# Kernel optimization log

Hardware: AMD Instinct MI355X
Metric: run time of the kernel (lower is better)

The kernel has to match this reference:

```python
import jax, jax.numpy as jnp
import numpy as np

N = 100000  # nodes
E = 1600000  # directed edges

_DIMS = [("eg1", 3, 160), ("eg2", 160, 80), ("eg3", 80, 40), ("eg4", 40, 20),
         ("el1", 20, 10), ("el2", 10, 3), ("dl1", 3, 10), ("dl2", 10, 20),
         ("dg1", 20, 40), ("dg2", 40, 80), ("dg3", 80, 160), ("dg4", 160, 3)]


def _lin_init(key, ci, co):
    s = 1.0 / np.sqrt(ci)
    kw, kb = jax.random.split(key)
    w = jax.random.uniform(kw, (ci, co), jnp.float32, -s, s)
    b = jax.random.uniform(kb, (co,), jnp.float32, -s, s)
    return w, b


def setup_inputs():
    key = jax.random.key(0)
    k0, k1, k2 = jax.random.split(key, 3)
    x = jax.random.normal(k0, (N, 3), jnp.float32)
    src = jax.random.randint(k1, (E,), 0, N)
    dst = jax.random.randint(k2, (E,), 0, N)
    edge_index = jnp.stack([src, dst])  # [2, E] int32 indices
    out = {"x": x, "edge_index": edge_index}
    for i, (name, ci, co) in enumerate(_DIMS):
        w, b = _lin_init(jax.random.fold_in(key, i + 10), ci, co)
        out[name + "_w"] = w
        out[name + "_b"] = b
    return out


def _gcn(x, w, b, src, dst, norm):
    # PyG GCNConv: linear transform, then symmetric-normalized scatter-add.
    h = x @ w
    agg = jax.ops.segment_sum(h[src] * norm[:, None], dst, num_segments=N)
    return agg + b


def reference(x, edge_index, eg1_w, eg1_b, eg2_w, eg2_b, eg3_w, eg3_b, eg4_w, eg4_b,
              el1_w, el1_b, el2_w, el2_b, dl1_w, dl1_b, dl2_w, dl2_b,
              dg1_w, dg1_b, dg2_w, dg2_b, dg3_w, dg3_b, dg4_w, dg4_b):
    loops = jnp.arange(N)
    src = jnp.concatenate([edge_index[0], loops])  # add self-loops (PyG default)
    dst = jnp.concatenate([edge_index[1], loops])
    deg = jax.ops.segment_sum(jnp.ones(src.shape[0], x.dtype), dst, num_segments=N)
    dis = jnp.where(deg > 0, jax.lax.rsqrt(deg), 0.0)
    norm = dis[src] * dis[dst]  # D^-1/2 A D^-1/2 edge weights
    relu = jax.nn.relu
    h = relu(_gcn(x, eg1_w, eg1_b, src, dst, norm))
    h = relu(_gcn(h, eg2_w, eg2_b, src, dst, norm))
    h = relu(_gcn(h, eg3_w, eg3_b, src, dst, norm))
    h = relu(_gcn(h, eg4_w, eg4_b, src, dst, norm))
    h = relu(h @ el1_w + el1_b)
    h = h @ el2_w + el2_b  # latent [N, 3]
    h = relu(h @ dl1_w + dl1_b)
    h = relu(h @ dl2_w + dl2_b)
    h = relu(_gcn(h, dg1_w, dg1_b, src, dst, norm))
    h = relu(_gcn(h, dg2_w, dg2_b, src, dst, norm))
    h = relu(_gcn(h, dg3_w, dg3_b, src, dst, norm))
    h = jnp.tanh(_gcn(h, dg4_w, dg4_b, src, dst, norm))
    return h
```

## Files before the change

### kernel.cpp

```cpp
#include <hip/hip_runtime.h>
#include <hip/hip_fp16.h>
#include <math.h>

#define BS 256
static constexpr int NN = 100000;
static constexpr int EE = 1600000;
static constexpr int BUCKET_SH = 7;
static constexpr int NBUCKET = (NN + 127) >> BUCKET_SH;
static constexpr int NB_PART = 256;
static constexpr int CHUNK = EE / NB_PART;
static constexpr int NP_ = NBUCKET * NB_PART;
static constexpr int SCAN_ELEMS = 1024;
static constexpr int NPB = (NP_ + SCAN_ELEMS - 1) / SCAN_ELEMS;

static inline int cdiv(long long a, int b) { return (int)((a + b - 1) / b); }

typedef _Float16 half8 __attribute__((ext_vector_type(8)));
typedef float f32x4 __attribute__((ext_vector_type(4)));

template <int ACT>
__device__ __forceinline__ float act_f(float v) {
    if (ACT == 1) return fmaxf(v, 0.0f);
    if (ACT == 2) return tanhf(v);
    return v;
}

__device__ __forceinline__ unsigned short h16(float v) {
    return __half_as_ushort(__float2half(v));
}
__device__ __forceinline__ unsigned pack2h(float a, float b) {
    return (unsigned)h16(a) | ((unsigned)h16(b) << 16);
}
__device__ __forceinline__ float4 cvt4h(uint2 r) {
    float2 fa = __half22float2(*(const __half2*)&r.x);
    float2 fb = __half22float2(*(const __half2*)&r.y);
    return make_float4(fa.x, fa.y, fb.x, fb.y);
}
__device__ __forceinline__ void acc8h(uint4 r, float4& a, float4& b) {
    float2 f0 = __half22float2(*(const __half2*)&r.x);
    float2 f1 = __half22float2(*(const __half2*)&r.y);
    float2 f2 = __half22float2(*(const __half2*)&r.z);
    float2 f3 = __half22float2(*(const __half2*)&r.w);
    a.x += f0.x; a.y += f0.y; a.z += f1.x; a.w += f1.y;
    b.x += f2.x; b.y += f2.y; b.z += f3.x; b.w += f3.y;
}
__device__ __forceinline__ void addrow8(uint4 r, float* h) {
    float2 f0 = __half22float2(*(const __half2*)&r.x);
    float2 f1 = __half22float2(*(const __half2*)&r.y);
    float2 f2 = __half22float2(*(const __half2*)&r.z);
    float2 f3 = __half22float2(*(const __half2*)&r.w);
    h[0] += f0.x; h[1] += f0.y; h[2] += f1.x; h[3] += f1.y;
    h[4] += f2.x; h[5] += f2.y; h[6] += f3.x; h[7] += f3.y;
}
__device__ __forceinline__ void addrow4(uint2 r, float* h) {
    float2 f0 = __half22float2(*(const __half2*)&r.x);
    float2 f1 = __half22float2(*(const __half2*)&r.y);
    h[0] += f0.x; h[1] += f0.y; h[2] += f1.x; h[3] += f1.y;
}

template <int OUTM>
__device__ __forceinline__ void store1(float* out, size_t idx, float v, float dn) {
    if (OUTM == 0) out[idx] = v;
    else if (OUTM == 1) out[idx] = v * dn;
    else if (OUTM == 2) ((unsigned short*)out)[idx] = h16(v * dn);
    else ((unsigned short*)out)[idx] = h16(v);
}

__global__ __launch_bounds__(256) void k_hist(const int* __restrict__ dst,
                                              int* __restrict__ part_cnt) {
    __shared__ int h[NBUCKET];
    int b = blockIdx.x;
    for (int j = threadIdx.x; j < NBUCKET; j += 256) h[j] = 0;
    __syncthreads();
    int e0 = b * CHUNK;
    for (int k = threadIdx.x; k < CHUNK; k += 256)
        atomicAdd(&h[dst[e0 + k] >> BUCKET_SH], 1);
    __syncthreads();
    for (int j = threadIdx.x; j < NBUCKET; j += 256)
        part_cnt[j * NB_PART + b] = h[j];
}

__global__ void k_scanA(const int* __restrict__ in, int* __restrict__ outp,
                        int* __restrict__ bsums) {
    __shared__ int lds[BS];
    int base = blockIdx.x * SCAN_ELEMS;
    int t = threadIdx.x;
    int v[4];
    int s = 0;
#pragma unroll
    for (int j = 0; j < 4; ++j) {
        int idx = base + t * 4 + j;
        v[j] = (idx < NP_) ? in[idx] : 0;
        s += v[j];
    }
    lds[t] = s;
    __syncthreads();
    for (int off = 1; off < BS; off <<= 1) {
        int add = (t >= off) ? lds[t - off] : 0;
        __syncthreads();
        lds[t] += add;
        __syncthreads();
    }
    int run = lds[t] - s;
    if (t == BS - 1) bsums[blockIdx.x] = lds[BS - 1];
#pragma unroll
    for (int j = 0; j < 4; ++j) {
        int idx = base + t * 4 + j;
        if (idx < NP_) outp[idx] = run;
        run += v[j];
    }
}

__global__ void k_scanB(int* __restrict__ bsums) {
    if (threadIdx.x == 0 && blockIdx.x == 0) {
        int acc = 0;
        for (int i = 0; i < NPB; ++i) {
            int t = bsums[i];
            bsums[i] = acc;
            acc += t;
        }
    }
}

__global__ void k_scanC(int* __restrict__ outp, const int* __restrict__ bsums,
                        int* __restrict__ bbase) {
    int i = blockIdx.x * BS + threadIdx.x;
    if (i < NP_) {
        int v = outp[i] + bsums[i / SCAN_ELEMS];
        outp[i] = v;
        if ((i & (NB_PART - 1)) == 0) bbase[i / NB_PART] = v;
    }
    if (i == 0) bbase[NBUCKET] = EE;
}

__global__ __launch_bounds__(256) void k_part(const int* __restrict__ src,
                                              const int* __restrict__ dst,
                                              const int* __restrict__ scan_out,
                                              unsigned* __restrict__ epb) {
    __shared__ int cur[NBUCKET];
    int b = blockIdx.x;
    for (int j = threadIdx.x; j < NBUCKET; j += 256) cur[j] = scan_out[j * NB_PART + b];
    __syncthreads();
    int e0 = b * CHUNK;
    for (int k = threadIdx.x; k < CHUNK; k += 256) {
        int e = e0 + k;
        int d = dst[e];
        int s = src[e];
        int pos = atomicAdd(&cur[d >> BUCKET_SH], 1);
        epb[pos] = ((unsigned)(d & ((1 << BUCKET_SH) - 1)) << 17) | (unsigned)s;
    }
}

__global__ __launch_bounds__(256) void k_fine2(const int* __restrict__ bbase,
                                               const unsigned* __restrict__ epb,
                                               int* __restrict__ eidx,
                                               int* __restrict__ rowptr,
                                               float* __restrict__ dis) {
    __shared__ int hcnt[1 << BUCKET_SH];
    __shared__ int hoff[1 << BUCKET_SH];
    int b = blockIdx.x;
    int n0 = b << BUCKET_SH;
    int nloc = min(1 << BUCKET_SH, NN - n0);
    int t = threadIdx.x;
    if (t < (1 << BUCKET_SH)) hcnt[t] = 0;
    __syncthreads();
    int es = bbase[b], ee = bbase[b + 1];
    for (int k = es + t; k < ee; k += 256) atomicAdd(&hcnt[epb[k] >> 17], 1);
    __syncthreads();
    if (t < (1 << BUCKET_SH)) hoff[t] = hcnt[t];
    __syncthreads();
    for (int off = 1; off < (1 << BUCKET_SH); off <<= 1) {
        int add = (t >= off && t < (1 << BUCKET_SH)) ? hoff[t - off] : 0;
        __syncthreads();
        if (t < (1 << BUCKET_SH)) hoff[t] += add;
        __syncthreads();
    }
    if (t < nloc) {
        int excl = hoff[t] - hcnt[t];
        rowptr[n0 + t] = es + excl;
        dis[n0 + t] = rsqrtf((float)(hcnt[t] + 1));
    }
    __syncthreads();
    if (t < (1 << BUCKET_SH)) hoff[t] = es + hoff[t] - hcnt[t];
    __syncthreads();
    for (int k = es + t; k < ee; k += 256) {
        unsigned p = epb[k];
        int pos = atomicAdd(&hoff[p >> 17], 1);
        eidx[pos] = (int)(p & 0x1FFFFu);
    }
    if (b == NBUCKET - 1 && t == 0) rowptr[NN] = EE;
}

template <int K, int N>
__device__ __forceinline__ void wconv(const float* __restrict__ w, _Float16* __restrict__ wh, int i) {
    constexpr int NT = (N + 15) / 16;
    constexpr int NPAD = NT * 16;
    int k = i / NPAD, n = i % NPAD;
    float v = (k < K && n < N) ? w[k * N + n] : 0.0f;
    wh[((size_t)(k >> 3) * NPAD + n) * 8 + (k & 7)] = (_Float16)v;
}

__global__ void k_wprep_all(const float* __restrict__ w1, const float* __restrict__ w2,
                            const float* __restrict__ w3, const float* __restrict__ w4,
                            _Float16* __restrict__ o1, _Float16* __restrict__ o2,
                            _Float16* __restrict__ o3, _Float16* __restrict__ o4) {
    int i = blockIdx.x * 256 + threadIdx.x;
    if (i < 12800) wconv<160, 80>(w1, o1, i);
    else if (i < 17408) wconv<80, 40>(w2, o2, i - 12800);
    else if (i < 22528) wconv<40, 80>(w3, o3, i - 17408);
    else if (i < 37888) wconv<80, 160>(w4, o4, i - 22528);
}

__global__ void k_gather3x(const float* __restrict__ x, const int* __restrict__ rowptr,
                           const int* __restrict__ eidx, const float* __restrict__ dis,
                           float* __restrict__ out) {
    int n = blockIdx.x * BS + threadIdx.x;
    if (n >= NN) return;
    float dn = dis[n];
    float a0 = x[(size_t)n * 3 + 0] * dn;
    float a1 = x[(size_t)n * 3 + 1] * dn;
    float a2 = x[(size_t)n * 3 + 2] * dn;
    int rs = rowptr[n], re = rowptr[n + 1];
    int k = rs;
    for (; k + 2 <= re; k += 2) {
        int s0 = eidx[k], s1 = eidx[k + 1];
        float d0 = dis[s0], d1 = dis[s1];
        const float* q0 = x + (size_t)s0 * 3;
        const float* q1 = x + (size_t)s1 * 3;
        a0 += q0[0] * d0 + q1[0] * d1;
        a1 += q0[1] * d0 + q1[1] * d1;
        a2 += q0[2] * d0 + q1[2] * d1;
    }
    for (; k < re; ++k) {
        int s = eidx[k];
        float ds = dis[s];
        const float* q = x + (size_t)s * 3;
        a0 += q[0] * ds; a1 += q[1] * ds; a2 += q[2] * ds;
    }
    float* op = out + (size_t)n * 3;
    op[0] = a0 * dn; op[1] = a1 * dn; op[2] = a2 * dn;
}

template <int ACT, bool HASB>
__global__ void k_gather3d(const float* __restrict__ g, const int* __restrict__ rowptr,
                           const int* __restrict__ eidx, const float* __restrict__ dis,
                           const float* __restrict__ b, float* __restrict__ out) {
    int n = blockIdx.x * BS + threadIdx.x;
    if (n >= NN) return;
    const float* gp = g + (size_t)n * 3;
    float a0 = gp[0], a1 = gp[1], a2 = gp[2];
    int rs = rowptr[n], re = rowptr[n + 1];
    int k = rs;
    for (; k + 4 <= re; k += 4) {
        const float* q0 = g + (size_t)eidx[k + 0] * 3;
        const float* q1 = g + (size_t)eidx[k + 1] * 3;
        const float* q2 = g + (size_t)eidx[k + 2] * 3;
        const float* q3 = g + (size_t)eidx[k + 3] * 3;
        a0 += (q0[0] + q1[0]) + (q2[0] + q3[0]);
        a1 += (q0[1] + q1[1]) + (q2[1] + q3[1]);
        a2 += (q0[2] + q1[2]) + (q2[2] + q3[2]);
    }
    for (; k < re; ++k) {
        const float* gq = g + (size_t)eidx[k] * 3;
        a0 += gq[0]; a1 += gq[1]; a2 += gq[2];
    }
    float dn = dis[n];
    a0 *= dn; a1 *= dn; a2 *= dn;
    if (HASB) { a0 += b[0]; a1 += b[1]; a2 += b[2]; }
    float* op = out + (size_t)n * 3;
    op[0] = act_f<ACT>(a0);
    op[1] = act_f<ACT>(a1);
    op[2] = act_f<ACT>(a2);
}

__global__ __launch_bounds__(256) void k_eg12(const float* __restrict__ a3,
                                              const float* __restrict__ w1,
                                              const float* __restrict__ b1,
                                              const _Float16* __restrict__ wh2,
                                              unsigned short* __restrict__ out,
                                              const float* __restrict__ dis) {
    constexpr int SP = 168;
    __shared__ _Float16 Al[64 * SP];
    __shared__ float xs[192];
    __shared__ float w1s[480];
    __shared__ float b1s[160];
    const int tid = threadIdx.x;
    const int n0 = blockIdx.x * 64;
    for (int i = tid; i < 192; i += 256) {
        int n = n0 + i / 3;
        xs[i] = (n < NN) ? a3[(size_t)n0 * 3 + i] : 0.0f;
    }
    for (int i = tid; i < 480; i += 256) w1s[i] = w1[i];
    if (tid < 160) b1s[tid] = b1[tid];
    __syncthreads();
    for (int i = tid; i < 64 * 160; i += 256) {
        int r = i / 160, c = i % 160;
        float v = b1s[c] + xs[r * 3 + 0] * w1s[c] + xs[r * 3 + 1] * w1s[160 + c] +
                  xs[r * 3 + 2] * w1s[320 + c];
        Al[r * SP + c] = (_Float16)fmaxf(v, 0.0f);
    }
    __syncthreads();
    const int wave = tid >> 6, lane = tid & 63;
    const int lm = lane & 15, quad = lane >> 4;
    f32x4 acc[5];
#pragma unroll
    for (int t = 0; t < 5; ++t) acc[t] = (f32x4){0.f, 0.f, 0.f, 0.f};
    const int arow = wave * 16 + lm;
#pragma unroll
    for (int kc = 0; kc < 5; ++kc) {
        half8 a = *(const half8*)&Al[arow * SP + kc * 32 + quad * 8];
#pragma unroll
        for (int t = 0; t < 5; ++t) {
            half8 bf = *(const half8*)&wh2[((size_t)(kc * 4 + quad) * 80 + t * 16 + lm) * 8];
            acc[t] = __builtin_amdgcn_mfma_f32_16x16x32_f16(a, bf, acc[t], 0, 0, 0);
        }
    }
#pragma unroll
    for (int r = 0; r < 4; ++r) {
        int orow = n0 + wave * 16 + quad * 4 + r;
        if (orow < NN) {
            float dn = dis[orow];
#pragma unroll
            for (int t = 0; t < 5; ++t) {
                int col = t * 16 + lm;
                out[(size_t)orow * 80 + col] = h16(acc[t][r] * dn);
            }
        }
    }
}

template <int CIN, int COUT, bool GHASB, int GACT, bool MHASB, int MACT, int OUTM>
__global__ __launch_bounds__(256) void k_gmfma(const unsigned short* __restrict__ gin,
                                               const int* __restrict__ rowptr,
                                               const int* __restrict__ eidx,
                                               const float* __restrict__ dis,
                                               const float* __restrict__ gbias,
                                               const _Float16* __restrict__ wh,
                                               const float* __restrict__ mbias,
                                               unsigned short* __restrict__ out) {
    static_assert(CIN % 8 == 0, "CIN%8");
    constexpr int V = CIN / 8;
    constexpr int SP = CIN + 8;
    constexpr int KP = (CIN + 31) & ~31;
    constexpr int KC = KP / 32;
    constexpr int NT = (COUT + 15) / 16;
    constexpr int NPAD = NT * 16;
    __shared__ _Float16 Al[64 * SP];
    const int tid = threadIdx.x;
    const int n0 = blockIdx.x * 64;
    const uint4* g4 = (const uint4*)gin;

    for (int i = tid; i < 64 * V; i += 256) {
        int r = i / V, c8 = i % V;
        int n = n0 + r;
        half8 hv = (half8)(_Float16)0;
        if (n < NN) {
            float4 aA = make_float4(0.f, 0.f, 0.f, 0.f);
            float4 aB = make_float4(0.f, 0.f, 0.f, 0.f);
            acc8h(g4[(size_t)n * V + c8], aA, aB);
            int rs = rowptr[n], re = rowptr[n + 1];
            int k = rs;
            for (; k + 4 <= re; k += 4) {
                int s0 = eidx[k + 0], s1 = eidx[k + 1], s2 = eidx[k + 2], s3 = eidx[k + 3];
                uint4 r0 = g4[(size_t)s0 * V + c8];
                uint4 r1 = g4[(size_t)s1 * V + c8];
                uint4 r2 = g4[(size_t)s2 * V + c8];
                uint4 r3 = g4[(size_t)s3 * V + c8];
                acc8h(r0, aA, aB);
                acc8h(r1, aA, aB);
                acc8h(r2, aA, aB);
                acc8h(r3, aA, aB);
            }
            for (; k < re; ++k) acc8h(g4[(size_t)eidx[k] * V + c8], aA, aB);
            float dn = dis[n];
            aA.x *= dn; aA.y *= dn; aA.z *= dn; aA.w *= dn;
            aB.x *= dn; aB.y *= dn; aB.z *= dn; aB.w *= dn;
            if (GHASB) {
                float4 b0 = ((const float4*)gbias)[c8 * 2 + 0];
                float4 b1 = ((const float4*)gbias)[c8 * 2 + 1];
                aA.x += b0.x; aA.y += b0.y; aA.z += b0.z; aA.w += b0.w;
                aB.x += b1.x; aB.y += b1.y; aB.z += b1.z; aB.w += b1.w;
            }
            if (GACT == 1) {
                aA.x = fmaxf(aA.x, 0.f); aA.y = fmaxf(aA.y, 0.f);
                aA.z = fmaxf(aA.z, 0.f); aA.w = fmaxf(aA.w, 0.f);
                aB.x = fmaxf(aB.x, 0.f); aB.y = fmaxf(aB.y, 0.f);
                aB.z = fmaxf(aB.z, 0.f); aB.w = fmaxf(aB.w, 0.f);
            }
            hv[0] = (_Float16)aA.x; hv[1] = (_Float16)aA.y;
            hv[2] = (_Float16)aA.z; hv[3] = (_Float16)aA.w;
            hv[4] = (_Float16)aB.x; hv[5] = (_Float16)aB.y;
            hv[6] = (_Float16)aB.z; hv[7] = (_Float16)aB.w;
        }
        *(half8*)&Al[r * SP + c8 * 8] = hv;
    }
    __syncthreads();

    const int wave = tid >> 6, lane = tid & 63;
    const int lm = lane & 15, quad = lane >> 4;
    f32x4 acc[NT];
#pragma unroll
    for (int t = 0; t < NT; ++t) acc[t] = (f32x4){0.f, 0.f, 0.f, 0.f};
    const int arow = wave * 16 + lm;
#pragma unroll
    for (int kc = 0; kc < KC; ++kc) {
        int k0 = kc * 32 + quad * 8;
        half8 a = (half8)(_Float16)0;
        if (k0 < CIN) a = *(const half8*)&Al[arow * SP + k0];
#pragma unroll
        for (int t = 0; t < NT; ++t) {
            half8 bf = *(const half8*)&wh[((size_t)(kc * 4 + quad) * NPAD + t * 16 + lm) * 8];
            acc[t] = __builtin_amdgcn_mfma_f32_16x16x32_f16(a, bf, acc[t], 0, 0, 0);
        }
    }
    float bb[NT];
#pragma unroll
    for (int t = 0; t < NT; ++t) {
        int col = t * 16 + lm;
        bb[t] = (MHASB && col < COUT) ? mbias[col] : 0.0f;
    }
#pragma unroll
    for (int r = 0; r < 4; ++r) {
        int orow = n0 + wave * 16 + quad * 4 + r;
        if (orow < NN) {
            float dn = (OUTM == 2) ? dis[orow] : 1.0f;
#pragma unroll
            for (int t = 0; t < NT; ++t) {
                int col = t * 16 + lm;
                if (col < COUT) {
                    float v = act_f<MACT>(acc[t][r] + bb[t]);
                    if (OUTM == 2) v *= dn;
                    out[(size_t)orow * COUT + col] = h16(v);
                }
            }
        }
    }
}

__global__ __launch_bounds__(256) void k_g40mm(const unsigned short* __restrict__ gin,
                                               const int* __restrict__ rowptr,
                                               const int* __restrict__ eidx,
                                               const float* __restrict__ dis,
                                               const float* __restrict__ gb,
                                               const float* __restrict__ w,
                                               unsigned short* __restrict__ out) {
    __shared__ float wS[800];
    __shared__ float bS[40];
    int tid = threadIdx.x;
    for (int i = tid; i < 800; i += 256) wS[i] = w[i];
    if (tid < 40) bS[tid] = gb[tid];
    __syncthreads();
    int n = blockIdx.x * 256 + tid;
    if (n >= NN) return;
    const uint4* g4 = (const uint4*)gin;
    float h[40];
#pragma unroll
    for (int i = 0; i < 40; ++i) h[i] = 0.0f;
#pragma unroll
    for (int c8 = 0; c8 < 5; ++c8) addrow8(g4[(size_t)n * 5 + c8], &h[c8 * 8]);
    int rs = rowptr[n], re = rowptr[n + 1];
    int k = rs;
    for (; k + 2 <= re; k += 2) {
        int s0 = eidx[k], s1 = eidx[k + 1];
#pragma unroll
        for (int c8 = 0; c8 < 5; ++c8) {
            uint4 r0 = g4[(size_t)s0 * 5 + c8];
            uint4 r1 = g4[(size_t)s1 * 5 + c8];
            addrow8(r0, &h[c8 * 8]);
            addrow8(r1, &h[c8 * 8]);
        }
    }
    for (; k < re; ++k) {
        int s = eidx[k];
#pragma unroll
        for (int c8 = 0; c8 < 5; ++c8) addrow8(g4[(size_t)s * 5 + c8], &h[c8 * 8]);
    }
    float dn = dis[n];
#pragma unroll
    for (int i = 0; i < 40; ++i) h[i] = fmaxf(h[i] * dn + bS[i], 0.0f);
    float z[20];
#pragma unroll
    for (int j = 0; j < 20; ++j) z[j] = 0.0f;
#pragma unroll
    for (int i = 0; i < 40; ++i) {
        float hv = h[i];
#pragma unroll
        for (int j = 0; j < 20; ++j) z[j] = fmaf(hv, wS[i * 20 + j], z[j]);
    }
    uint2* gp = (uint2*)out + (size_t)n * 5;
#pragma unroll
    for (int q = 0; q < 5; ++q) {
        uint2 u;
        u.x = pack2h(z[q * 4 + 0] * dn, z[q * 4 + 1] * dn);
        u.y = pack2h(z[q * 4 + 2] * dn, z[q * 4 + 3] * dn);
        gp[q] = u;
    }
}

__global__ __launch_bounds__(256) void k_g20_latent(const unsigned short* __restrict__ gin,
                                                    const int* __restrict__ rowptr,
                                                    const int* __restrict__ eidx,
                                                    const float* __restrict__ dis,
                                                    const float* __restrict__ gb,
                                                    const float* __restrict__ el1_w, const float* __restrict__ el1_b,
                                                    const float* __restrict__ el2_w, const float* __restrict__ el2_b,
                                                    const float* __restrict__ dl1_w, const float* __restrict__ dl1_b,
                                                    const float* __restrict__ dl2_w, const float* __restrict__ dl2_b,
                                                    unsigned short* __restrict__ out) {
    __shared__ float w1[200], b1[10], w2[30], b2[3], w3[30], b3[10], w4[200], b4[20], bg[20];
    int t = threadIdx.x;
    if (t < 200) w1[t] = el1_w[t];
    if (t < 10) b1[t] = el1_b[t];
    if (t < 30) w2[t] = el2_w[t];
    if (t < 3) b2[t] = el2_b[t];
    if (t < 30) w3[t] = dl1_w[t];
    if (t < 10) b3[t] = dl1_b[t];
    if (t < 200) w4[t] = dl2_w[t];
    if (t < 20) b4[t] = dl2_b[t];
    if (t >= 220 && t < 240) bg[t - 220] = gb[t - 220];
    __syncthreads();
    int n = blockIdx.x * 256 + t;
    if (n >= NN) return;
    const uint2* g2 = (const uint2*)gin;
    float h0[20];
#pragma unroll
    for (int i = 0; i < 20; ++i) h0[i] = 0.0f;
#pragma unroll
    for (int c4 = 0; c4 < 5; ++c4) addrow4(g2[(size_t)n * 5 + c4], &h0[c4 * 4]);
    int rs = rowptr[n], re = rowptr[n + 1];
    int k = rs;
    for (; k + 4 <= re; k += 4) {
        int s0 = eidx[k], s1 = eidx[k + 1], s2 = eidx[k + 2], s3 = eidx[k + 3];
#pragma unroll
        for (int c4 = 0; c4 < 5; ++c4) {
            uint2 r0 = g2[(size_t)s0 * 5 + c4];
            uint2 r1 = g2[(size_t)s1 * 5 + c4];
            uint2 r2 = g2[(size_t)s2 * 5 + c4];
            uint2 r3 = g2[(size_t)s3 * 5 + c4];
            addrow4(r0, &h0[c4 * 4]);
            addrow4(r1, &h0[c4 * 4]);
            addrow4(r2, &h0[c4 * 4]);
            addrow4(r3, &h0[c4 * 4]);
        }
    }
    for (; k < re; ++k) {
        int s = eidx[k];
#pragma unroll
        for (int c4 = 0; c4 < 5; ++c4) addrow4(g2[(size_t)s * 5 + c4], &h0[c4 * 4]);
    }
    float dn = dis[n];
#pragma unroll
    for (int i = 0; i < 20; ++i) h0[i] = fmaxf(h0[i] * dn + bg[i], 0.0f);
    float a1[10];
#pragma unroll
    for (int j = 0; j < 10; ++j) {
        float s = b1[j];
#pragma unroll
        for (int i = 0; i < 20; ++i) s = fmaf(h0[i], w1[i * 10 + j], s);
        a1[j] = fmaxf(s, 0.0f);
    }
    float a2[3];
#pragma unroll
    for (int j = 0; j < 3; ++j) {
        float s = b2[j];
#pragma unroll
        for (int i = 0; i < 10; ++i) s = fmaf(a1[i], w2[i * 3 + j], s);
        a2[j] = s;
    }
    float a3[10];
#pragma unroll
    for (int j = 0; j < 10; ++j) {
        float s = b3[j];
#pragma unroll
        for (int i = 0; i < 3; ++i) s = fmaf(a2[i], w3[i * 10 + j], s);
        a3[j] = fmaxf(s, 0.0f);
    }
    uint2* gp = (uint2*)out + (size_t)n * 5;
#pragma unroll
    for (int v = 0; v < 5; ++v) {
        float o[4];
#pragma unroll
        for (int q = 0; q < 4; ++q) {
            int j = v * 4 + q;
            float s = b4[j];
#pragma unroll
            for (int i = 0; i < 10; ++i) s = fmaf(a3[i], w4[i * 20 + j], s);
            o[q] = fmaxf(s, 0.0f) * dn;
        }
        uint2 u;
        u.x = pack2h(o[0], o[1]);
        u.y = pack2h(o[2], o[3]);
        gp[v] = u;
    }
}

__global__ __launch_bounds__(256) void k_g20_mm(const unsigned short* __restrict__ gin,
                                                const int* __restrict__ rowptr,
                                                const int* __restrict__ eidx,
                                                const float* __restrict__ dis,
                                                const float* __restrict__ w,
                                                const float* __restrict__ b,
                                                unsigned short* __restrict__ out) {
    __shared__ float wS[800];
    __shared__ float bS[40];
    int tid = threadIdx.x;
    for (int i = tid; i < 800; i += 256) wS[i] = w[i];
    if (tid < 40) bS[tid] = b[tid];
    __syncthreads();
    int n = blockIdx.x * 256 + tid;
    if (n >= NN) return;
    const uint2* g2 = (const uint2*)gin;
    float h[20];
#pragma unroll
    for (int i = 0; i < 20; ++i) h[i] = 0.0f;
#pragma unroll
    for (int c4 = 0; c4 < 5; ++c4) addrow4(g2[(size_t)n * 5 + c4], &h[c4 * 4]);
    int rs = rowptr[n], re = rowptr[n + 1];
    int k = rs;
    for (; k + 4 <= re; k += 4) {
        int s0 = eidx[k], s1 = eidx[k + 1], s2 = eidx[k + 2], s3 = eidx[k + 3];
#pragma unroll
        for (int c4 = 0; c4 < 5; ++c4) {
            uint2 r0 = g2[(size_t)s0 * 5 + c4];
            uint2 r1 = g2[(size_t)s1 * 5 + c4];
            uint2 r2 = g2[(size_t)s2 * 5 + c4];
            uint2 r3 = g2[(size_t)s3 * 5 + c4];
            addrow4(r0, &h[c4 * 4]);
            addrow4(r1, &h[c4 * 4]);
            addrow4(r2, &h[c4 * 4]);
            addrow4(r3, &h[c4 * 4]);
        }
    }
    for (; k < re; ++k) {
        int s = eidx[k];
#pragma unroll
        for (int c4 = 0; c4 < 5; ++c4) addrow4(g2[(size_t)s * 5 + c4], &h[c4 * 4]);
    }
    float dn = dis[n];
#pragma unroll
    for (int i = 0; i < 20; ++i) h[i] *= dn;
    float z[40];
#pragma unroll
    for (int j = 0; j < 40; ++j) z[j] = bS[j];
#pragma unroll
    for (int i = 0; i < 20; ++i) {
        float hv = h[i];
#pragma unroll
        for (int j = 0; j < 40; ++j) z[j] = fmaf(hv, wS[i * 40 + j], z[j]);
    }
    uint2* gp = (uint2*)out + (size_t)n * 10;
#pragma unroll
    for (int q = 0; q < 10; ++q) {
        float z0 = fmaxf(z[q * 4 + 0], 0.f) * dn;
        float z1 = fmaxf(z[q * 4 + 1], 0.f) * dn;
        float z2 = fmaxf(z[q * 4 + 2], 0.f) * dn;
        float z3 = fmaxf(z[q * 4 + 3], 0.f) * dn;
        uint2 u;
        u.x = pack2h(z0, z1);
        u.y = pack2h(z2, z3);
        gp[q] = u;
    }
}

template <int CIN, int COUT, int ACT, bool HASB, int OUTM, bool INH>
__global__ void k_mm_vec(const float* __restrict__ x, const float* __restrict__ w,
                         const float* __restrict__ b, float* __restrict__ out,
                         const float* __restrict__ dis) {
    static_assert(CIN % 4 == 0, "CIN%4");
    constexpr int TM = 8;
    constexpr int CIN4 = CIN / 4;
    constexpr int RG = NN / TM;
    int i = blockIdx.x * BS + threadIdx.x;
    if (i >= RG * COUT) return;
    int c = i % COUT;
    int n0 = (i / COUT) * TM;
    float acc[TM];
    float bb = HASB ? b[c] : 0.0f;
#pragma unroll
    for (int r = 0; r < TM; ++r) acc[r] = bb;
    const float4* x4 = (const float4*)x;
    const uint2* xh = (const uint2*)x;
    for (int k = 0; k < CIN4; ++k) {
        float w0 = w[(4 * k + 0) * COUT + c];
        float w1 = w[(4 * k + 1) * COUT + c];
        float w2 = w[(4 * k + 2) * COUT + c];
        float w3 = w[(4 * k + 3) * COUT + c];
#pragma unroll
        for (int r = 0; r < TM; ++r) {
            float4 xv;
            if (INH) xv = cvt4h(xh[(size_t)(n0 + r) * CIN4 + k]);
            else xv = x4[(size_t)(n0 + r) * CIN4 + k];
            acc[r] = fmaf(xv.x, w0, fmaf(xv.y, w1, fmaf(xv.z, w2, fmaf(xv.w, w3, acc[r]))));
        }
    }
#pragma unroll
    for (int r = 0; r < TM; ++r) {
        int row = n0 + r;
        float dn = (OUTM == 1 || OUTM == 2) ? dis[row] : 0.0f;
        store1<OUTM>(out, (size_t)row * COUT + c, act_f<ACT>(acc[r]), dn);
    }
}

extern "C" void kernel_launch(void* const* d_in, const int* in_sizes, int n_in,
                              void* d_out, int out_size, void* d_ws, size_t ws_size,
                              hipStream_t stream) {
    const float* x = (const float*)d_in[0];
    const int* ei = (const int*)d_in[1];
    const int* src = ei;
    const int* dst = ei + EE;
    const float* eg1_w = (const float*)d_in[2];  const float* eg1_b = (const float*)d_in[3];
    const float* eg2_w = (const float*)d_in[4];  const float* eg2_b = (const float*)d_in[5];
    const float* eg3_w = (const float*)d_in[6];  const float* eg3_b = (const float*)d_in[7];
    const float* eg4_w = (const float*)d_in[8];  const float* eg4_b = (const float*)d_in[9];
    const float* el1_w = (const float*)d_in[10]; const float* el1_b = (const float*)d_in[11];
    const float* el2_w = (const float*)d_in[12]; const float* el2_b = (const float*)d_in[13];
    const float* dl1_w = (const float*)d_in[14]; const float* dl1_b = (const float*)d_in[15];
    const float* dl2_w = (const float*)d_in[16]; const float* dl2_b = (const float*)d_in[17];
    const float* dg1_w = (const float*)d_in[18]; const float* dg1_b = (const float*)d_in[19];
    const float* dg2_w = (const float*)d_in[20]; const float* dg2_b = (const float*)d_in[21];
    const float* dg3_w = (const float*)d_in[22]; const float* dg3_b = (const float*)d_in[23];
    const float* dg4_w = (const float*)d_in[24]; const float* dg4_b = (const float*)d_in[25];
    float* out = (float*)d_out;

    char* ws = (char*)d_ws;
    size_t off = 0;
    auto alloc = [&](size_t bytes) {
        void* p = ws + off;
        off += (bytes + 15) & ~(size_t)15;
        return p;
    };
    int* part_cnt = (int*)alloc(sizeof(int) * NP_);
    int* scan_out = (int*)alloc(sizeof(int) * NP_);
    int* bsums    = (int*)alloc(sizeof(int) * NPB);
    int* bbase    = (int*)alloc(sizeof(int) * (NBUCKET + 1));
    int* rowptr   = (int*)alloc(sizeof(int) * (NN + 1));
    float* dis    = (float*)alloc(sizeof(float) * NN);
    int* eidx     = (int*)alloc(sizeof(int) * EE);
    unsigned* epb = (unsigned*)alloc(sizeof(unsigned) * EE);
    float* A3     = (float*)alloc(sizeof(float) * 3 * (size_t)NN);
    unsigned short* GA = (unsigned short*)alloc(sizeof(unsigned short) * 80 * (size_t)NN);
    unsigned short* GB = (unsigned short*)alloc(sizeof(unsigned short) * 80 * (size_t)NN);
    unsigned short* B160 = (unsigned short*)alloc(sizeof(unsigned short) * 160 * (size_t)NN);
    _Float16* whEg2 = (_Float16*)alloc(sizeof(_Float16) * 12800);
    _Float16* whEg3 = (_Float16*)alloc(sizeof(_Float16) * 4608);
    _Float16* whDg2 = (_Float16*)alloc(sizeof(_Float16) * 5120);
    _Float16* whDg3 = (_Float16*)alloc(sizeof(_Float16) * 15360);

    k_hist<<<NB_PART, 256, 0, stream>>>(dst, part_cnt);
    k_scanA<<<NPB, BS, 0, stream>>>(part_cnt, scan_out, bsums);
    k_scanB<<<1, 64, 0, stream>>>(bsums);
    k_scanC<<<cdiv(NP_, BS), BS, 0, stream>>>(scan_out, bsums, bbase);
    k_part<<<NB_PART, 256, 0, stream>>>(src, dst, scan_out, epb);
    k_fine2<<<NBUCKET, 256, 0, stream>>>(bbase, epb, eidx, rowptr, dis);

    k_wprep_all<<<cdiv(37888, 256), 256, 0, stream>>>(eg2_w, eg3_w, dg2_w, dg3_w,
                                                      whEg2, whEg3, whDg2, whDg3);

    k_gather3x<<<cdiv(NN, BS), BS, 0, stream>>>(x, rowptr, eidx, dis, A3);
    k_eg12<<<cdiv(NN, 64), 256, 0, stream>>>(A3, eg1_w, eg1_b, whEg2, GA, dis);
    k_gmfma<80, 40, true, 1, false, 0, 2><<<cdiv(NN, 64), 256, 0, stream>>>(
        GA, rowptr, eidx, dis, eg2_b, whEg3, nullptr, GB);
    k_g40mm<<<cdiv(NN, 256), 256, 0, stream>>>(GB, rowptr, eidx, dis, eg3_b, eg4_w, GA);
    k_g20_latent<<<cdiv(NN, 256), 256, 0, stream>>>(GA, rowptr, eidx, dis, eg4_b,
        el1_w, el1_b, el2_w, el2_b, dl1_w, dl1_b, dl2_w, dl2_b, GB);
    k_g20_mm<<<cdiv(NN, 256), 256, 0, stream>>>(GB, rowptr, eidx, dis, dg1_w, dg1_b, GA);
    k_gmfma<40, 80, false, 0, true, 1, 2><<<cdiv(NN, 64), 256, 0, stream>>>(
        GA, rowptr, eidx, dis, nullptr, whDg2, dg2_b, GB);
    k_gmfma<80, 160, false, 0, true, 1, 3><<<cdiv(NN, 64), 256, 0, stream>>>(
        GB, rowptr, eidx, dis, nullptr, whDg3, dg3_b, B160);
    k_mm_vec<160, 3, 0, false, 1, true><<<cdiv((NN / 8) * 3LL, BS), BS, 0, stream>>>(
        (const float*)B160, dg4_w, nullptr, A3, dis);
    k_gather3d<2, true><<<cdiv(NN, BS), BS, 0, stream>>>(A3, rowptr, eidx, dis, dg4_b, out);
}
```

Measured before the change: 538.6 us.

## Split fused gather+MFMA kernels into separate gather and matmul kernels

Replaces the fused k_gmfma kernel, which gathered neighbor rows into shared memory and then ran an MFMA matmul, with two kernels. A thread-per-8-channel gather kernel writes the aggregated fp16 features to global memory, and a standalone MFMA matmul kernel reads them back. The aim is better gather parallelism and occupancy, since the fused kernel had few threads per block doing the gather and the matmul waited on a barrier. The cost is an extra global round trip of the intermediate activations and extra kernel launches.

```diff
diff --git a/kernel.cpp b/kernel.cpp
--- a/kernel.cpp
+++ b/kernel.cpp
@@ -273,6 +273,114 @@
     op[2] = act_f<ACT>(a2);
 }
 
+template <int C, int ACT, bool HASB>
+__global__ void k_gatherw(const unsigned short* __restrict__ g, const int* __restrict__ rowptr,
+                          const int* __restrict__ eidx, const float* __restrict__ dis,
+                          const float* __restrict__ b, unsigned short* __restrict__ out) {
+    static_assert(C % 8 == 0, "C%8");
+    constexpr int V = C / 8;
+    int t = blockIdx.x * BS + threadIdx.x;
+    if (t >= NN * V) return;
+    int n = t / V, v = t % V;
+    const uint4* g4 = (const uint4*)g;
+    float4 accA = make_float4(0.f, 0.f, 0.f, 0.f);
+    float4 accB = make_float4(0.f, 0.f, 0.f, 0.f);
+    acc8h(g4[(size_t)n * V + v], accA, accB);
+    int rs = rowptr[n], re = rowptr[n + 1];
+    int k = rs;
+    for (; k + 4 <= re; k += 4) {
+        int s0 = eidx[k + 0], s1 = eidx[k + 1], s2 = eidx[k + 2], s3 = eidx[k + 3];
+        uint4 r0 = g4[(size_t)s0 * V + v];
+        uint4 r1 = g4[(size_t)s1 * V + v];
+        uint4 r2 = g4[(size_t)s2 * V + v];
+        uint4 r3 = g4[(size_t)s3 * V + v];
+        acc8h(r0, accA, accB);
+        acc8h(r1, accA, accB);
+        acc8h(r2, accA, accB);
+        acc8h(r3, accA, accB);
+    }
+    for (; k < re; ++k) {
+        acc8h(g4[(size_t)eidx[k] * V + v], accA, accB);
+    }
+    float dn = dis[n];
+    accA.x *= dn; accA.y *= dn; accA.z *= dn; accA.w *= dn;
+    accB.x *= dn; accB.y *= dn; accB.z *= dn; accB.w *= dn;
+    if (HASB) {
+        float4 b0 = ((const float4*)b)[v * 2 + 0];
+        float4 b1 = ((const float4*)b)[v * 2 + 1];
+        accA.x += b0.x; accA.y += b0.y; accA.z += b0.z; accA.w += b0.w;
+        accB.x += b1.x; accB.y += b1.y; accB.z += b1.z; accB.w += b1.w;
+    }
+    accA.x = act_f<ACT>(accA.x); accA.y = act_f<ACT>(accA.y);
+    accA.z = act_f<ACT>(accA.z); accA.w = act_f<ACT>(accA.w);
+    accB.x = act_f<ACT>(accB.x); accB.y = act_f<ACT>(accB.y);
+    accB.z = act_f<ACT>(accB.z); accB.w = act_f<ACT>(accB.w);
+    uint4 u;
+    u.x = pack2h(accA.x, accA.y);
+    u.y = pack2h(accA.z, accA.w);
+    u.z = pack2h(accB.x, accB.y);
+    u.w = pack2h(accB.z, accB.w);
+    ((uint4*)out)[(size_t)n * V + v] = u;
+}
+
+template <int K, int N, int ACT, bool HASB, int OUTM>
+__global__ __launch_bounds__(256) void k_mfma(const unsigned short* __restrict__ x,
+                                              const _Float16* __restrict__ wh,
+                                              const float* __restrict__ bias,
+                                              unsigned short* __restrict__ out,
+                                              const float* __restrict__ dis) {
+    static_assert(K % 8 == 0, "K%8");
+    constexpr int KP = (K + 31) & ~31;
+    constexpr int KC = KP / 32;
+    constexpr int NT = (N + 15) / 16;
+    constexpr int NPAD = NT * 16;
+    const int wid = blockIdx.x * 4 + (threadIdx.x >> 6);
+    const int lane = threadIdx.x & 63;
+    const int lm = lane & 15;
+    const int quad = lane >> 4;
+    const int arow = wid * 16 + lm;
+
+    f32x4 acc[NT];
+#pragma unroll
+    for (int t = 0; t < NT; ++t) acc[t] = (f32x4){0.f, 0.f, 0.f, 0.f};
+
+    const _Float16* xr = (const _Float16*)x + (size_t)arow * K;
+#pragma unroll
+    for (int kc = 0; kc < KC; ++kc) {
+        int k0 = kc * 32 + quad * 8;
+        half8 a = (half8)(_Float16)0;
+        if (arow < NN && k0 < K) a = *(const half8*)(xr + k0);
+#pragma unroll
+        for (int t = 0; t < NT; ++t) {
+            half8 bf = *(const half8*)&wh[((size_t)(kc * 4 + quad) * NPAD + t * 16 + lm) * 8];
+            acc[t] = __builtin_amdgcn_mfma_f32_16x16x32_f16(a, bf, acc[t], 0, 0, 0);
+        }
+    }
+
+    float bb[NT];
+#pragma unroll
+    for (int t = 0; t < NT; ++t) {
+        int col = t * 16 + lm;
+        bb[t] = (HASB && col < N) ? bias[col] : 0.0f;
+    }
+#pragma unroll
+    for (int r = 0; r < 4; ++r) {
+        int orow = wid * 16 + quad * 4 + r;
+        if (orow < NN) {
+            float dn = (OUTM == 2) ? dis[orow] : 1.0f;
+#pragma unroll
+            for (int t = 0; t < NT; ++t) {
+                int col = t * 16 + lm;
+                if (col < N) {
+                    float v = act_f<ACT>(acc[t][r] + bb[t]);
+                    if (OUTM == 2) v *= dn;
+                    out[(size_t)orow * N + col] = h16(v);
+                }
+            }
+        }
+    }
+}
+
 __global__ __launch_bounds__(256) void k_eg12(const float* __restrict__ a3,
                                               const float* __restrict__ w1,
                                               const float* __restrict__ b1,
@@ -324,114 +432,6 @@
             for (int t = 0; t < 5; ++t) {
                 int col = t * 16 + lm;
                 out[(size_t)orow * 80 + col] = h16(acc[t][r] * dn);
-            }
-        }
-    }
-}
-
-template <int CIN, int COUT, bool GHASB, int GACT, bool MHASB, int MACT, int OUTM>
-__global__ __launch_bounds__(256) void k_gmfma(const unsigned short* __restrict__ gin,
-                                               const int* __restrict__ rowptr,
-                                               const int* __restrict__ eidx,
-                                               const float* __restrict__ dis,
-                                               const float* __restrict__ gbias,
-                                               const _Float16* __restrict__ wh,
-                                               const float* __restrict__ mbias,
-                                               unsigned short* __restrict__ out) {
-    static_assert(CIN % 8 == 0, "CIN%8");
-    constexpr int V = CIN / 8;
-    constexpr int SP = CIN + 8;
-    constexpr int KP = (CIN + 31) & ~31;
-    constexpr int KC = KP / 32;
-    constexpr int NT = (COUT + 15) / 16;
-    constexpr int NPAD = NT * 16;
-    __shared__ _Float16 Al[64 * SP];
-    const int tid = threadIdx.x;
-    const int n0 = blockIdx.x * 64;
-    const uint4* g4 = (const uint4*)gin;
-
-    for (int i = tid; i < 64 * V; i += 256) {
-        int r = i / V, c8 = i % V;
-        int n = n0 + r;
-        half8 hv = (half8)(_Float16)0;
-        if (n < NN) {
-            float4 aA = make_float4(0.f, 0.f, 0.f, 0.f);
-            float4 aB = make_float4(0.f, 0.f, 0.f, 0.f);
-            acc8h(g4[(size_t)n * V + c8], aA, aB);
-            int rs = rowptr[n], re = rowptr[n + 1];
-            int k = rs;
-            for (; k + 4 <= re; k += 4) {
-                int s0 = eidx[k + 0], s1 = eidx[k + 1], s2 = eidx[k + 2], s3 = eidx[k + 3];
-                uint4 r0 = g4[(size_t)s0 * V + c8];
-                uint4 r1 = g4[(size_t)s1 * V + c8];
-                uint4 r2 = g4[(size_t)s2 * V + c8];
-                uint4 r3 = g4[(size_t)s3 * V + c8];
-                acc8h(r0, aA, aB);
-                acc8h(r1, aA, aB);
-                acc8h(r2, aA, aB);
-                acc8h(r3, aA, aB);
-            }
-            for (; k < re; ++k) acc8h(g4[(size_t)eidx[k] * V + c8], aA, aB);
-            float dn = dis[n];
-            aA.x *= dn; aA.y *= dn; aA.z *= dn; aA.w *= dn;
-            aB.x *= dn; aB.y *= dn; aB.z *= dn; aB.w *= dn;
-            if (GHASB) {
-                float4 b0 = ((const float4*)gbias)[c8 * 2 + 0];
-                float4 b1 = ((const float4*)gbias)[c8 * 2 + 1];
-                aA.x += b0.x; aA.y += b0.y; aA.z += b0.z; aA.w += b0.w;
-                aB.x += b1.x; aB.y += b1.y; aB.z += b1.z; aB.w += b1.w;
-            }
-            if (GACT == 1) {
-                aA.x = fmaxf(aA.x, 0.f); aA.y = fmaxf(aA.y, 0.f);
-                aA.z = fmaxf(aA.z, 0.f); aA.w = fmaxf(aA.w, 0.f);
-                aB.x = fmaxf(aB.x, 0.f); aB.y = fmaxf(aB.y, 0.f);
-                aB.z = fmaxf(aB.z, 0.f); aB.w = fmaxf(aB.w, 0.f);
-            }
-            hv[0] = (_Float16)aA.x; hv[1] = (_Float16)aA.y;
-            hv[2] = (_Float16)aA.z; hv[3] = (_Float16)aA.w;
-            hv[4] = (_Float16)aB.x; hv[5] = (_Float16)aB.y;
-            hv[6] = (_Float16)aB.z; hv[7] = (_Float16)aB.w;
-        }
-        *(half8*)&Al[r * SP + c8 * 8] = hv;
-    }
-    __syncthreads();
-
-    const int wave = tid >> 6, lane = tid & 63;
-    const int lm = lane & 15, quad = lane >> 4;
-    f32x4 acc[NT];
-#pragma unroll
-    for (int t = 0; t < NT; ++t) acc[t] = (f32x4){0.f, 0.f, 0.f, 0.f};
-    const int arow = wave * 16 + lm;
-#pragma unroll
-    for (int kc = 0; kc < KC; ++kc) {
-        int k0 = kc * 32 + quad * 8;
-        half8 a = (half8)(_Float16)0;
-        if (k0 < CIN) a = *(const half8*)&Al[arow * SP + k0];
-#pragma unroll
-        for (int t = 0; t < NT; ++t) {
-            half8 bf = *(const half8*)&wh[((size_t)(kc * 4 + quad) * NPAD + t * 16 + lm) * 8];
-            acc[t] = __builtin_amdgcn_mfma_f32_16x16x32_f16(a, bf, acc[t], 0, 0, 0);
-        }
-    }
-    float bb[NT];
-#pragma unroll
-    for (int t = 0; t < NT; ++t) {
-        int col = t * 16 + lm;
-        bb[t] = (MHASB && col < COUT) ? mbias[col] : 0.0f;
-    }
-#pragma unroll
-    for (int r = 0; r < 4; ++r) {
-        int orow = n0 + wave * 16 + quad * 4 + r;
-        if (orow < NN) {
-            float dn = (OUTM == 2) ? dis[orow] : 1.0f;
-#pragma unroll
-            for (int t = 0; t < NT; ++t) {
-                int col = t * 16 + lm;
-                if (col < COUT) {
-                    float v = act_f<MACT>(acc[t][r] + bb[t]);
-                    if (OUTM == 2) v *= dn;
-                    out[(size_t)orow * COUT + col] = h16(v);
-                }
             }
         }
     }
@@ -758,16 +758,16 @@
 
     k_gather3x<<<cdiv(NN, BS), BS, 0, stream>>>(x, rowptr, eidx, dis, A3);
     k_eg12<<<cdiv(NN, 64), 256, 0, stream>>>(A3, eg1_w, eg1_b, whEg2, GA, dis);
-    k_gmfma<80, 40, true, 1, false, 0, 2><<<cdiv(NN, 64), 256, 0, stream>>>(
-        GA, rowptr, eidx, dis, eg2_b, whEg3, nullptr, GB);
-    k_g40mm<<<cdiv(NN, 256), 256, 0, stream>>>(GB, rowptr, eidx, dis, eg3_b, eg4_w, GA);
-    k_g20_latent<<<cdiv(NN, 256), 256, 0, stream>>>(GA, rowptr, eidx, dis, eg4_b,
-        el1_w, el1_b, el2_w, el2_b, dl1_w, dl1_b, dl2_w, dl2_b, GB);
-    k_g20_mm<<<cdiv(NN, 256), 256, 0, stream>>>(GB, rowptr, eidx, dis, dg1_w, dg1_b, GA);
-    k_gmfma<40, 80, false, 0, true, 1, 2><<<cdiv(NN, 64), 256, 0, stream>>>(
-        GA, rowptr, eidx, dis, nullptr, whDg2, dg2_b, GB);
-    k_gmfma<80, 160, false, 0, true, 1, 3><<<cdiv(NN, 64), 256, 0, stream>>>(
-        GB, rowptr, eidx, dis, nullptr, whDg3, dg3_b, B160);
+    k_gatherw<80, 1, true><<<cdiv(NN * 10LL, BS), BS, 0, stream>>>(GA, rowptr, eidx, dis, eg2_b, GB);
+    k_mfma<80, 40, 0, false, 2><<<cdiv(NN, 64), 256, 0, stream>>>(GB, whEg3, nullptr, GA, dis);
+    k_g40mm<<<cdiv(NN, 256), 256, 0, stream>>>(GA, rowptr, eidx, dis, eg3_b, eg4_w, GB);
+    k_g20_latent<<<cdiv(NN, 256), 256, 0, stream>>>(GB, rowptr, eidx, dis, eg4_b,
+        el1_w, el1_b, el2_w, el2_b, dl1_w, dl1_b, dl2_w, dl2_b, GA);
+    k_g20_mm<<<cdiv(NN, 256), 256, 0, stream>>>(GA, rowptr, eidx, dis, dg1_w, dg1_b, GB);
+    k_gatherw<40, 0, false><<<cdiv(NN * 5LL, BS), BS, 0, stream>>>(GB, rowptr, eidx, dis, nullptr, GA);
+    k_mfma<40, 80, 1, true, 2><<<cdiv(NN, 64), 256, 0, stream>>>(GA, whDg2, dg2_b, GB, dis);
+    k_gatherw<80, 0, false><<<cdiv(NN * 10LL, BS), BS, 0, stream>>>(GB, rowptr, eidx, dis, nullptr, GA);
+    k_mfma<80, 160, 1, true, 3><<<cdiv(NN, 64), 256, 0, stream>>>(GA, whDg3, dg3_b, B160, nullptr);
     k_mm_vec<160, 3, 0, false, 1, true><<<cdiv((NN / 8) * 3LL, BS), BS, 0, stream>>>(
         (const float*)B160, dg4_w, nullptr, A3, dis);
     k_gather3d<2, true><<<cdiv(NN, BS), BS, 0, stream>>>(A3, rowptr, eidx, dis, dg4_b, out);
```

Result: no change. 543.5 us (+0.9%).
